# Kernel tuning notes

Measured on AMD Instinct MI355X. Metric: run time of the kernel, lower is better.

## Reference

```python
import jax, jax.numpy as jnp
import numpy as np

B, T = 32, 1024
IN_SIZE, SENSORY, HIDDEN, MOTOR, OUT_SIZE = 512, 512, 1024, 512, 512


def setup_inputs() -> dict:
    key = jax.random.key(0)
    ks = jax.random.split(key, 12)

    def glorot(k, shape):
        fan_in = shape[-1]
        return (jax.random.normal(k, shape, jnp.float32) / np.sqrt(fan_in)).astype(jnp.float32)

    inputs = jax.random.normal(ks[0], (B, T, IN_SIZE), jnp.float32)
    timespans = jnp.ones((B, T), jnp.float32)
    init_hidden = jnp.zeros((B, HIDDEN), jnp.float32)

    # input_mapping: Linear(input_size -> sensory_size)
    W_in = glorot(ks[1], (SENSORY, IN_SIZE))
    b_in = jnp.zeros((SENSORY,), jnp.float32)
    # LTC cell parameters
    W_x = glorot(ks[2], (HIDDEN, SENSORY))
    W_h = glorot(ks[3], (HIDDEN, HIDDEN))
    b_cell = jnp.zeros((HIDDEN,), jnp.float32)
    tau = jax.random.uniform(ks[4], (HIDDEN,), jnp.float32, 0.5, 2.0)  # positive time constants
    A = jax.random.normal(ks[5], (HIDDEN,), jnp.float32)  # target/bias vector of ODE
    # output_mapping: Linear(motor_size -> output_size)
    W_out = glorot(ks[6], (OUT_SIZE, MOTOR))
    b_out = jnp.zeros((OUT_SIZE,), jnp.float32)

    return {
        "inputs": inputs, "timespans": timespans, "init_hidden": init_hidden,
        "W_in": W_in, "b_in": b_in,
        "W_x": W_x, "W_h": W_h, "b_cell": b_cell, "tau": tau, "A": A,
        "W_out": W_out, "b_out": b_out,
    }


def reference(inputs, timespans, init_hidden, W_in, b_in, W_x, W_h, b_cell, tau, A, W_out, b_out):
    # embedding = vmap(input_mapping)(inputs): [B,T,SENSORY]
    emb = jnp.einsum('bti,si->bts', inputs, W_in) + b_in
    emb_t = jnp.swapaxes(emb, 0, 1)          # [T,B,SENSORY] (scan over time)
    ts_t = jnp.swapaxes(timespans, 0, 1)     # [T,B]
    inv_tau = 1.0 / tau

    def step(h, xs):
        ts, x = xs                            # ts: [B], x: [B,SENSORY]
        # liquid-time-constant fused semi-implicit Euler step
        f = jax.nn.sigmoid(x @ W_x.T + h @ W_h.T + b_cell)   # [B,HIDDEN]
        tsb = ts[:, None]
        h_new = (h + tsb * f * A) / (1.0 + tsb * (inv_tau + f))
        return h_new, h_new

    last_state, hidden_seq = jax.lax.scan(step, init_hidden, (ts_t, emb_t))  # hidden_seq: [T,B,HIDDEN]
    motor_seq = hidden_seq[..., :MOTOR]                                       # [T,B,MOTOR]
    out_seq = jnp.einsum('tbm,om->tbo', motor_seq, W_out) + b_out             # [T,B,OUT]
    return jnp.swapaxes(out_seq, 0, 1), last_state                            # ([B,T,OUT], [B,HIDDEN])
```

## Files before the change

kernel.cpp:

```cpp
#include <hip/hip_runtime.h>
#include <math.h>

#define B_SZ   32
#define T_SZ   1024
#define IN_SZ  512
#define SEN    512
#define HID    1024
#define MOT    512
#define OUT_SZ 512

#define NBLK   32
#define JSL    32
#define K2     512
#define WPAD   516

typedef __fp16  f16x8 __attribute__((ext_vector_type(8)));
typedef float   f32x4 __attribute__((ext_vector_type(4)));

__device__ inline uint32_t pk16(float a, float b) {
  auto p = __builtin_amdgcn_cvt_pkrtz(a, b);
  return __builtin_bit_cast(uint32_t, p);
}

template<bool TB>
__global__ __launch_bounds__(256) void gemm_tiled(
    const float* __restrict__ A, const float* __restrict__ Bm,
    const float* __restrict__ bias, float* __restrict__ C,
    int M, int N, int K, int lda,
    int P, long long S1, long long S2)
{
  __shared__ float As[16][64 + 1];
  __shared__ float Bs[16][64 + 1];
  const int tid = threadIdx.x;
  const int n0 = blockIdx.x * 64;
  const int r0 = blockIdx.y * 64;
  const int ty = tid / 16;
  const int tx = tid % 16;

  float acc[4][4] = {};

  for (int k0 = 0; k0 < K; k0 += 16) {
    {
      const int kk = tid % 16, m0 = tid / 16;
      #pragma unroll
      for (int i = 0; i < 4; i++) {
        const int m = m0 + i * 16;
        As[kk][m] = A[(long long)(r0 + m) * lda + k0 + kk];
      }
    }
    if (TB) {
      const int kk = tid % 16, nl0 = tid / 16;
      #pragma unroll
      for (int i = 0; i < 4; i++) {
        const int n = nl0 + i * 16;
        Bs[kk][n] = Bm[(long long)(n0 + n) * K + k0 + kk];
      }
    } else {
      const int nl = tid % 64, kk0 = tid / 64;
      #pragma unroll
      for (int i = 0; i < 4; i++) {
        const int kk = kk0 + i * 4;
        Bs[kk][nl] = Bm[(long long)(k0 + kk) * N + n0 + nl];
      }
    }
    __syncthreads();

    #pragma unroll
    for (int kk = 0; kk < 16; kk++) {
      float av[4], bv[4];
      #pragma unroll
      for (int i = 0; i < 4; i++) av[i] = As[kk][ty * 4 + i];
      #pragma unroll
      for (int j = 0; j < 4; j++) bv[j] = Bs[kk][tx * 4 + j];
      #pragma unroll
      for (int i = 0; i < 4; i++)
        #pragma unroll
        for (int j = 0; j < 4; j++)
          acc[i][j] += av[i] * bv[j];
    }
    __syncthreads();
  }

  #pragma unroll
  for (int i = 0; i < 4; i++) {
    const int r = r0 + ty * 4 + i;
    const long long base = (long long)(r % P) * S1 + (long long)(r / P) * S2;
    #pragma unroll
    for (int j = 0; j < 4; j++) {
      const int c = n0 + tx * 4 + j;
      float v = acc[i][j];
      if (bias) v += bias[c];
      C[base + c] = v;
    }
  }
}

__global__ __launch_bounds__(256) void gemm_mfma(
    const uint32_t* __restrict__ A16, const uint32_t* __restrict__ B16,
    const float* __restrict__ bias, float* __restrict__ C,
    int K2w, int P, long long S1, long long S2)
{
  __shared__ uint32_t Al[128 * 20];
  __shared__ uint32_t Bl[128 * 20];
  const int tid  = threadIdx.x;
  const int r0   = blockIdx.y * 128;
  const int c0   = blockIdx.x * 128;
  const int wv   = tid >> 6, lane = tid & 63;
  const int wrow = wv >> 1, wcol = wv & 1;
  const int row16 = lane & 15, kg = lane >> 4;

  const int srow = tid >> 1;
  const int scol = (tid & 1) * 8;

  f32x4 acc[4][4];
  #pragma unroll
  for (int a = 0; a < 4; ++a)
    #pragma unroll
    for (int b = 0; b < 4; ++b) acc[a][b] = (f32x4){0.f, 0.f, 0.f, 0.f};

  const int nkt = K2w / 16;
  for (int kt = 0; kt < nkt; ++kt) {
    const uint32_t* ag = A16 + (size_t)(r0 + srow) * K2w + kt * 16 + scol;
    const uint32_t* bg = B16 + (size_t)(c0 + srow) * K2w + kt * 16 + scol;
    *(uint4*)&Al[srow * 20 + scol]     = *(const uint4*)ag;
    *(uint4*)&Al[srow * 20 + scol + 4] = *(const uint4*)(ag + 4);
    *(uint4*)&Bl[srow * 20 + scol]     = *(const uint4*)bg;
    *(uint4*)&Bl[srow * 20 + scol + 4] = *(const uint4*)(bg + 4);
    __syncthreads();

    uint4 af[4], bf[4];
    #pragma unroll
    for (int f = 0; f < 4; ++f) {
      af[f] = *(const uint4*)&Al[(wrow * 64 + f * 16 + row16) * 20 + kg * 4];
      bf[f] = *(const uint4*)&Bl[(wcol * 64 + f * 16 + row16) * 20 + kg * 4];
    }
    #pragma unroll
    for (int fr = 0; fr < 4; ++fr)
      #pragma unroll
      for (int fc = 0; fc < 4; ++fc)
        acc[fr][fc] = __builtin_amdgcn_mfma_f32_16x16x32_f16(
            __builtin_bit_cast(f16x8, af[fr]), __builtin_bit_cast(f16x8, bf[fc]),
            acc[fr][fc], 0, 0, 0);
    __syncthreads();
  }

  #pragma unroll
  for (int fr = 0; fr < 4; ++fr) {
    #pragma unroll
    for (int reg = 0; reg < 4; ++reg) {
      const int rg = r0 + wrow * 64 + fr * 16 + kg * 4 + reg;
      const long long base = (long long)(rg % P) * S1 + (long long)(rg / P) * S2;
      #pragma unroll
      for (int fc = 0; fc < 4; ++fc) {
        const int cg = c0 + wcol * 64 + fc * 16 + row16;
        C[base + cg] = acc[fr][fc][reg] + (bias ? bias[cg] : 0.f);
      }
    }
  }
}

__global__ void bias_eff_kernel(const float* __restrict__ Wx,
                                const float* __restrict__ b_in,
                                const float* __restrict__ b_cell,
                                float* __restrict__ bias_eff)
{
  const int h = blockIdx.x * 256 + threadIdx.x;
  float s = b_cell[h];
  for (int k = 0; k < SEN; k++) s += Wx[h * SEN + k] * b_in[k];
  bias_eff[h] = s;
}

__global__ __launch_bounds__(256) void pack16_kernel(
    const float* __restrict__ in, uint32_t* __restrict__ outp)
{
  const size_t idx = (size_t)blockIdx.x * 256 + threadIdx.x;
  const float2 v = *(const float2*)(in + idx * 2);
  outp[idx] = pk16(v.x, v.y);
}

__global__ __launch_bounds__(256) void init_hx_kernel(
    const float* __restrict__ init_h, uint32_t* __restrict__ hx0)
{
  const int idx = blockIdx.x * 256 + threadIdx.x;
  const int b  = idx >> 9;
  const int j2 = idx & 511;
  const float2 v = *(const float2*)(init_h + (size_t)b * HID + 2 * j2);
  hx0[(j2 >> 2) * 128 + b * 4 + (j2 & 3)] = pk16(v.x, v.y);
}

__global__ __launch_bounds__(256, 1) void scan_x_kernel(
    const float* __restrict__ init_h,
    const uint32_t* __restrict__ Wp16,
    const float* __restrict__ pre,
    const float* __restrict__ tsp,
    const float* __restrict__ Avec,
    const float* __restrict__ tau,
    uint32_t* __restrict__ hseq16,
    uint32_t* __restrict__ hx,
    uint32_t* __restrict__ flags,
    float* __restrict__ last_state)
{
  __shared__ uint32_t w_lds[JSL * WPAD];

  const int bk   = blockIdx.x;
  const int tid  = threadIdx.x;
  const int wv   = tid >> 6;
  const int lane = tid & 63;
  const int qr   = wv >> 1;
  const int qc   = wv & 1;
  const int row16 = lane & 15;
  const int kg    = lane >> 4;

  const int j_loc  = qc * 16 + row16;
  const int j_glob = bk * JSL + j_loc;
  const int b0     = qr * 16 + kg * 4;

  {
    const uint32_t* src = Wp16 + (size_t)bk * JSL * K2;
    for (int i = tid; i < JSL * K2; i += 256)
      w_lds[(i >> 9) * WPAD + (i & (K2 - 1))] = src[i];
  }

  const float a_j  = Avec[j_glob];
  const float it_j = 1.f / tau[j_glob];
  float h_old[4];
  #pragma unroll
  for (int r = 0; r < 4; ++r) h_old[r] = init_h[(b0 + r) * HID + j_glob];

  float prevC[4], tsC[4];
  #pragma unroll
  for (int r = 0; r < 4; ++r) {
    prevC[r] = pre[(size_t)(b0 + r) * HID + j_glob];
    tsC[r]   = tsp[(b0 + r) * T_SZ + 0];
  }

  __syncthreads();

  const uint32_t* brow = &w_lds[j_loc * WPAD];
  const int ab2 = (qr * 16 + row16) * 2;
  const int pub_base = (j_glob >> 3) * 128 + ((j_glob >> 1) & 3);

  for (int t = 0; t < T_SZ; ++t) {
    if (t > 0) {
      if (tid < 64) {
        const uint32_t tgt = (uint32_t)t;
        while (__hip_atomic_load(&flags[(tid & 31) * 16],
                                 __ATOMIC_RELAXED, __HIP_MEMORY_SCOPE_AGENT) < tgt)
          __builtin_amdgcn_s_sleep(1);
      }
      __syncthreads();
    }

    const unsigned long long* hxr =
        (const unsigned long long*)(hx + (t & 1) * (B_SZ * K2));
    unsigned long long a64[64];
    #pragma unroll
    for (int kk = 0; kk < 32; ++kk) {
      const size_t base = (size_t)(kk * 4 + kg) * 64 + ab2;
      a64[2 * kk]     = __hip_atomic_load(&hxr[base],
                          __ATOMIC_RELAXED, __HIP_MEMORY_SCOPE_AGENT);
      a64[2 * kk + 1] = __hip_atomic_load(&hxr[base + 1],
                          __ATOMIC_RELAXED, __HIP_MEMORY_SCOPE_AGENT);
    }

    f32x4 acc = {0.f, 0.f, 0.f, 0.f};
    #pragma unroll
    for (int kk = 0; kk < 32; ++kk) {
      const uint4 av = make_uint4((uint32_t)a64[2 * kk],
                                  (uint32_t)(a64[2 * kk] >> 32),
                                  (uint32_t)a64[2 * kk + 1],
                                  (uint32_t)(a64[2 * kk + 1] >> 32));
      const uint4 bv = *(const uint4*)(brow + kk * 16 + kg * 4);
      acc = __builtin_amdgcn_mfma_f32_16x16x32_f16(
          __builtin_bit_cast(f16x8, av), __builtin_bit_cast(f16x8, bv),
          acc, 0, 0, 0);
    }

    float hn[4];
    #pragma unroll
    for (int r = 0; r < 4; ++r) {
      const float z = acc[r] + prevC[r];
      const float f = 1.f / (1.f + __expf(-z));
      hn[r] = (h_old[r] + tsC[r] * f * a_j) / (1.f + tsC[r] * (it_j + f));
      h_old[r] = hn[r];
    }

    uint32_t pkv[4];
    #pragma unroll
    for (int r = 0; r < 4; ++r) {
      const float partner = __shfl_xor(hn[r], 1);
      pkv[r] = pk16(hn[r], partner);
    }

    uint32_t* hxw = hx + ((t + 1) & 1) * (B_SZ * K2);
    if ((row16 & 1) == 0) {
      #pragma unroll
      for (int r = 0; r < 4; ++r)
        __hip_atomic_store(&hxw[pub_base + (b0 + r) * 4], pkv[r],
                           __ATOMIC_RELAXED, __HIP_MEMORY_SCOPE_AGENT);
    }

    __syncthreads();

    if (tid == 0)
      __hip_atomic_store(&flags[bk * 16], (uint32_t)(t + 1),
                         __ATOMIC_RELAXED, __HIP_MEMORY_SCOPE_AGENT);

    if (bk < 16 && (row16 & 1) == 0) {
      #pragma unroll
      for (int r = 0; r < 4; ++r)
        hseq16[(size_t)t * (B_SZ * 256) + (b0 + r) * 256 + (j_glob >> 1)] = pkv[r];
    }
    const int tn = (t + 1 < T_SZ) ? t + 1 : t;
    #pragma unroll
    for (int r = 0; r < 4; ++r) {
      prevC[r] = pre[(size_t)tn * (B_SZ * HID) + (b0 + r) * HID + j_glob];
      tsC[r]   = tsp[(b0 + r) * T_SZ + tn];
    }
  }

  #pragma unroll
  for (int r = 0; r < 4; ++r)
    last_state[(b0 + r) * HID + j_glob] = h_old[r];
}

extern "C" void kernel_launch(void* const* d_in, const int* in_sizes, int n_in,
                              void* d_out, int out_size, void* d_ws, size_t ws_size,
                              hipStream_t stream)
{
  const float* inputs    = (const float*)d_in[0];
  const float* timespans = (const float*)d_in[1];
  const float* init_h    = (const float*)d_in[2];
  const float* W_in      = (const float*)d_in[3];
  const float* b_in      = (const float*)d_in[4];
  const float* W_x       = (const float*)d_in[5];
  const float* W_h       = (const float*)d_in[6];
  const float* b_cell    = (const float*)d_in[7];
  const float* tau       = (const float*)d_in[8];
  const float* A         = (const float*)d_in[9];
  const float* W_out     = (const float*)d_in[10];
  const float* b_out     = (const float*)d_in[11];
  float* out = (float*)d_out;

  float*    ws     = (float*)d_ws;
  float*    pre    = ws;
  uint32_t* hseq16 = (uint32_t*)(pre + (size_t)T_SZ * B_SZ * HID);
  uint32_t* in16   = hseq16 + (size_t)T_SZ * B_SZ * 256;
  float*    Wxi    = (float*)(in16 + (size_t)B_SZ * T_SZ * 256);
  uint32_t* wxi16  = (uint32_t*)(Wxi + (size_t)HID * IN_SZ);
  uint32_t* wh16   = wxi16 + (size_t)HID * (IN_SZ / 2);
  uint32_t* wout16 = wh16 + (size_t)HID * K2;
  float*    beff   = (float*)(wout16 + (size_t)OUT_SZ * (MOT / 2));
  uint32_t* hx     = (uint32_t*)(beff + HID);
  uint32_t* flags  = hx + 2 * B_SZ * K2;

  gemm_tiled<false><<<dim3(IN_SZ / 64, HID / 64), 256, 0, stream>>>(
      W_x, W_in, nullptr, Wxi, HID, IN_SZ, SEN, SEN,
      1 << 30, (long long)IN_SZ, 0LL);

  bias_eff_kernel<<<HID / 256, 256, 0, stream>>>(W_x, b_in, b_cell, beff);

  pack16_kernel<<<(B_SZ * T_SZ * IN_SZ / 2) / 256, 256, 0, stream>>>(inputs, in16);
  pack16_kernel<<<(HID * IN_SZ / 2) / 256, 256, 0, stream>>>(Wxi, wxi16);
  pack16_kernel<<<(HID * HID / 2) / 256, 256, 0, stream>>>(W_h, wh16);
  pack16_kernel<<<(OUT_SZ * MOT / 2) / 256, 256, 0, stream>>>(W_out, wout16);

  gemm_mfma<<<dim3(HID / 128, (B_SZ * T_SZ) / 128), 256, 0, stream>>>(
      in16, wxi16, beff, pre, IN_SZ / 2,
      T_SZ, (long long)B_SZ * HID, (long long)HID);

  init_hx_kernel<<<(B_SZ * K2) / 256, 256, 0, stream>>>(init_h, hx);
  (void)hipMemsetAsync(flags, 0, NBLK * 16 * sizeof(uint32_t), stream);

  {
    const uint32_t* wh16c = (const uint32_t*)wh16;
    float* last_state = out + (size_t)B_SZ * T_SZ * OUT_SZ;
    void* args[] = {
      (void*)&init_h, (void*)&wh16c, (void*)&pre, (void*)&timespans,
      (void*)&A, (void*)&tau, (void*)&hseq16, (void*)&hx, (void*)&flags,
      (void*)&last_state
    };
    (void)hipLaunchCooperativeKernel((void*)scan_x_kernel, dim3(NBLK), dim3(256),
                                     args, 0, stream);
  }

  gemm_mfma<<<dim3(OUT_SZ / 128, (B_SZ * T_SZ) / 128), 256, 0, stream>>>(
      hseq16, wout16, b_out, out, MOT / 2,
      B_SZ, (long long)T_SZ * OUT_SZ, (long long)OUT_SZ);
}
```

Before: 3.949 ms.

## Replace per-step flag barrier with tagged 64-bit hidden-state words

Each published half2 hidden value is widened to a 64-bit word whose upper half carries the timestep tag. Consumers poll the data directly, in four k-chunks, until every tag matches, which removes the flag spin loop and the block-wide barrier before each step's matvec. A fallback to the old flag wait after many spins preserves progress. The cost is doubled load traffic for the hidden-state exchange and reuse of the Wxi workspace region for the buffers.

```diff
diff --git a/kernel.cpp b/kernel.cpp
--- a/kernel.cpp
+++ b/kernel.cpp
@@ -13,6 +13,7 @@
 #define JSL    32
 #define K2     512
 #define WPAD   516
+#define PARSZ  16384
 
 typedef __fp16  f16x8 __attribute__((ext_vector_type(8)));
 typedef float   f32x4 __attribute__((ext_vector_type(4)));
@@ -179,13 +180,13 @@
 }
 
 __global__ __launch_bounds__(256) void init_hx_kernel(
-    const float* __restrict__ init_h, uint32_t* __restrict__ hx0)
+    const float* __restrict__ init_h, unsigned long long* __restrict__ hx0)
 {
   const int idx = blockIdx.x * 256 + threadIdx.x;
   const int b  = idx >> 9;
   const int j2 = idx & 511;
   const float2 v = *(const float2*)(init_h + (size_t)b * HID + 2 * j2);
-  hx0[(j2 >> 2) * 128 + b * 4 + (j2 & 3)] = pk16(v.x, v.y);
+  hx0[(j2 >> 2) * 128 + b * 4 + (j2 & 3)] = (unsigned long long)pk16(v.x, v.y);
 }
 
 __global__ __launch_bounds__(256, 1) void scan_x_kernel(
@@ -196,7 +197,7 @@
     const float* __restrict__ Avec,
     const float* __restrict__ tau,
     uint32_t* __restrict__ hseq16,
-    uint32_t* __restrict__ hx,
+    unsigned long long* __restrict__ hx,
     uint32_t* __restrict__ flags,
     float* __restrict__ last_state)
 {
@@ -237,43 +238,58 @@
   __syncthreads();
 
   const uint32_t* brow = &w_lds[j_loc * WPAD];
-  const int ab2 = (qr * 16 + row16) * 2;
+  const int ab4 = (qr * 16 + row16) * 4;
   const int pub_base = (j_glob >> 3) * 128 + ((j_glob >> 1) & 3);
 
   for (int t = 0; t < T_SZ; ++t) {
-    if (t > 0) {
-      if (tid < 64) {
-        const uint32_t tgt = (uint32_t)t;
-        while (__hip_atomic_load(&flags[(tid & 31) * 16],
-                                 __ATOMIC_RELAXED, __HIP_MEMORY_SCOPE_AGENT) < tgt)
+    const unsigned long long* hxr = hx + (size_t)(t & 1) * PARSZ;
+    const uint32_t tg = (uint32_t)t;
+    bool trusted = false;
+
+    f32x4 acc = {0.f, 0.f, 0.f, 0.f};
+
+    #pragma unroll
+    for (int kb = 0; kb < 4; ++kb) {
+      unsigned long long a[32];
+      int spin = 0;
+      while (true) {
+        #pragma unroll
+        for (int i = 0; i < 8; ++i) {
+          const int kk = kb * 8 + i;
+          const size_t base = (size_t)(kk * 4 + kg) * 128 + ab4;
+          #pragma unroll
+          for (int w = 0; w < 4; ++w)
+            a[i * 4 + w] = __hip_atomic_load(&hxr[base + w],
+                             __ATOMIC_RELAXED, __HIP_MEMORY_SCOPE_AGENT);
+        }
+        if (trusted) break;
+        bool ok = true;
+        #pragma unroll
+        for (int i = 0; i < 32; ++i)
+          ok &= ((uint32_t)(a[i] >> 32) == tg);
+        if (__all(ok)) break;
+        if (++spin > 2048) {
+          while (true) {
+            const uint32_t v = __hip_atomic_load(&flags[(lane & 31) * 16],
+                                 __ATOMIC_RELAXED, __HIP_MEMORY_SCOPE_AGENT);
+            if (__all(v >= tg)) break;
+            __builtin_amdgcn_s_sleep(8);
+          }
+          trusted = true;
+        } else {
           __builtin_amdgcn_s_sleep(1);
-      }
-      __syncthreads();
-    }
-
-    const unsigned long long* hxr =
-        (const unsigned long long*)(hx + (t & 1) * (B_SZ * K2));
-    unsigned long long a64[64];
-    #pragma unroll
-    for (int kk = 0; kk < 32; ++kk) {
-      const size_t base = (size_t)(kk * 4 + kg) * 64 + ab2;
-      a64[2 * kk]     = __hip_atomic_load(&hxr[base],
-                          __ATOMIC_RELAXED, __HIP_MEMORY_SCOPE_AGENT);
-      a64[2 * kk + 1] = __hip_atomic_load(&hxr[base + 1],
-                          __ATOMIC_RELAXED, __HIP_MEMORY_SCOPE_AGENT);
-    }
-
-    f32x4 acc = {0.f, 0.f, 0.f, 0.f};
-    #pragma unroll
-    for (int kk = 0; kk < 32; ++kk) {
-      const uint4 av = make_uint4((uint32_t)a64[2 * kk],
-                                  (uint32_t)(a64[2 * kk] >> 32),
-                                  (uint32_t)a64[2 * kk + 1],
-                                  (uint32_t)(a64[2 * kk + 1] >> 32));
-      const uint4 bv = *(const uint4*)(brow + kk * 16 + kg * 4);
-      acc = __builtin_amdgcn_mfma_f32_16x16x32_f16(
-          __builtin_bit_cast(f16x8, av), __builtin_bit_cast(f16x8, bv),
-          acc, 0, 0, 0);
+        }
+      }
+      #pragma unroll
+      for (int i = 0; i < 8; ++i) {
+        const int kk = kb * 8 + i;
+        const uint4 av = make_uint4((uint32_t)a[i * 4 + 0], (uint32_t)a[i * 4 + 1],
+                                    (uint32_t)a[i * 4 + 2], (uint32_t)a[i * 4 + 3]);
+        const uint4 bv = *(const uint4*)(brow + kk * 16 + kg * 4);
+        acc = __builtin_amdgcn_mfma_f32_16x16x32_f16(
+            __builtin_bit_cast(f16x8, av), __builtin_bit_cast(f16x8, bv),
+            acc, 0, 0, 0);
+      }
     }
 
     float hn[4];
@@ -292,11 +308,13 @@
       pkv[r] = pk16(hn[r], partner);
     }
 
-    uint32_t* hxw = hx + ((t + 1) & 1) * (B_SZ * K2);
+    unsigned long long* hxw = hx + (size_t)((t + 1) & 1) * PARSZ;
+    const unsigned long long tagv = ((unsigned long long)(t + 1)) << 32;
     if ((row16 & 1) == 0) {
       #pragma unroll
       for (int r = 0; r < 4; ++r)
-        __hip_atomic_store(&hxw[pub_base + (b0 + r) * 4], pkv[r],
+        __hip_atomic_store(&hxw[pub_base + (b0 + r) * 4],
+                           tagv | (unsigned long long)pkv[r],
                            __ATOMIC_RELAXED, __HIP_MEMORY_SCOPE_AGENT);
     }
 
@@ -351,8 +369,9 @@
   uint32_t* wh16   = wxi16 + (size_t)HID * (IN_SZ / 2);
   uint32_t* wout16 = wh16 + (size_t)HID * K2;
   float*    beff   = (float*)(wout16 + (size_t)OUT_SZ * (MOT / 2));
-  uint32_t* hx     = (uint32_t*)(beff + HID);
-  uint32_t* flags  = hx + 2 * B_SZ * K2;
+
+  unsigned long long* hx    = (unsigned long long*)Wxi;
+  uint32_t*           flags = (uint32_t*)(hx + 2 * PARSZ);
 
   gemm_tiled<false><<<dim3(IN_SZ / 64, HID / 64), 256, 0, stream>>>(
       W_x, W_in, nullptr, Wxi, HID, IN_SZ, SEN, SEN,
@@ -369,8 +388,10 @@
       in16, wxi16, beff, pre, IN_SZ / 2,
       T_SZ, (long long)B_SZ * HID, (long long)HID);
 
+  (void)hipMemsetAsync(hx, 0,
+                       2 * PARSZ * sizeof(unsigned long long) +
+                       NBLK * 16 * sizeof(uint32_t), stream);
   init_hx_kernel<<<(B_SZ * K2) / 256, 256, 0, stream>>>(init_h, hx);
-  (void)hipMemsetAsync(flags, 0, NBLK * 16 * sizeof(uint32_t), stream);
 
   {
     const uint32_t* wh16c = (const uint32_t*)wh16;
```

New measurement: 6.970 ms. 76.5% more time.
